# Kernel tuning notes

Hardware: AMD Instinct MI355X
Metric: run time of the kernel (lower is better)

Reference implementation:

```python
import jax, jax.numpy as jnp
import numpy as np

B, T, C, H = 8, 1024, 512, 8


def setup_inputs() -> dict:
    key = jax.random.key(0)
    k1, k2, k3, k4 = jax.random.split(key, 4)
    x = jax.random.normal(k1, (B, T, C), jnp.float32)
    q = jax.random.normal(k2, (B, T, C), jnp.float32)
    W_kv = jax.random.normal(k3, (C, 2 * C), jnp.float32) * 0.02
    W_proj = jax.random.normal(k4, (C, C), jnp.float32) * 0.02
    return {"x": x, "q": q, "W_kv": W_kv, "W_proj": W_proj}


def reference(x, q, W_kv, W_proj):
    B, T, C = x.shape
    H = 8
    D = C // H
    T2 = T // 2
    # kv projection (nn.Linear, no bias)
    kv = x @ W_kv                      # [B,T,2C]
    k, v = kv[..., :C], kv[..., C:]
    # 7 batch-dim rolls of the first half, then reinterpret [7,B,T2,C] -> [B,7*T2,C]
    # (exactly what torch.stack(...).view(B,-1,C) does on the contiguous buffer)
    sk = jnp.stack([jnp.roll(k[:, :T2], i, axis=0) for i in range(7)]).reshape(B, -1, C)
    sv = jnp.stack([jnp.roll(v[:, :T2], i, axis=0) for i in range(7)]).reshape(B, -1, C)
    k = jnp.concatenate((sk, k), axis=1)   # [B, S, C], S = 7*T2 + T
    v = jnp.concatenate((sv, v), axis=1)
    qh = q.reshape(B, T, H, D).transpose(0, 2, 1, 3)    # [B,H,T,D]
    kh = k.reshape(B, -1, H, D).transpose(0, 2, 1, 3)   # [B,H,S,D]
    vh = v.reshape(B, -1, H, D).transpose(0, 2, 1, 3)   # [B,H,S,D]
    scale = 1.0 / jnp.sqrt(jnp.float32(D))
    # NOTE: the torch module passes attn_mask=None to SDPA, so attention is unmasked
    scores = jnp.einsum('bhld,bhsd->bhls', qh, kh) * scale
    attn = jax.nn.softmax(scores, axis=-1)
    y = jnp.einsum('bhls,bhsd->bhld', attn, vh)
    y = y.transpose(0, 2, 1, 3).reshape(B, T, C)
    return y @ W_proj
```

## Files before the change

kernel.cpp:

```cpp
#include <hip/hip_runtime.h>

typedef __bf16 bf16;
typedef bf16 bf16x8 __attribute__((ext_vector_type(8)));
typedef bf16 bf16x4 __attribute__((ext_vector_type(4)));
typedef float f32x4 __attribute__((ext_vector_type(4)));
typedef float f32x16 __attribute__((ext_vector_type(16)));
typedef unsigned int u32;

#define DEV_INLINE __device__ __forceinline__

DEV_INLINE f32x4 mfma16(bf16x8 a, bf16x8 b, f32x4 c) {
    return __builtin_amdgcn_mfma_f32_16x16x32_bf16(a, b, c, 0, 0, 0);
}
DEV_INLINE f32x16 mfma32(bf16x8 a, bf16x8 b, f32x16 c) {
    return __builtin_amdgcn_mfma_f32_32x32x16_bf16(a, b, c, 0, 0, 0);
}

#define GLD16(gp, lp) __builtin_amdgcn_global_load_lds( \
    (const __attribute__((address_space(1))) void*)(gp), \
    (__attribute__((address_space(3))) void*)(lp), 16, 0, 0)

__global__ void transpose_cast_kernel(const float* __restrict__ in, bf16* __restrict__ out,
                                      int K, int N) {
    int idx = blockIdx.x * blockDim.x + threadIdx.x;
    if (idx < K * N) {
        int n = idx / K, k = idx - n * K;
        out[idx] = (bf16)in[k * N + n];
    }
}

__launch_bounds__(256, 2)
__global__ void gemm_kv_kernel(const float* __restrict__ A,
                               const bf16* __restrict__ Bt,
                               bf16* __restrict__ Kout,
                               bf16* __restrict__ Vt)
{
    __shared__ bf16 As[128][32];
    __shared__ bf16 Bs[128][32];
    const int bm = blockIdx.x, bn = blockIdx.y;
    const int tid = threadIdx.x;
    const int lane = tid & 63, w = tid >> 6;
    const int wm = (w >> 1) * 64, wn = (w & 1) * 64;
    const int lr = lane & 15, kg = lane >> 4;

    const f32x4 fz = {0.f, 0.f, 0.f, 0.f};
    f32x4 acc[4][4];
    for (int i = 0; i < 4; ++i)
        for (int j = 0; j < 4; ++j) acc[i][j] = fz;

    const int srow = tid >> 2, sc4 = tid & 3;

    for (int k0 = 0; k0 < 512; k0 += 32) {
        __syncthreads();
        for (int rr = 0; rr < 2; ++rr) {
            int row = srow + rr * 64;
            const float* ap = A + (size_t)(bm * 128 + row) * 512 + k0 + (sc4 << 3);
            f32x4 a0 = *reinterpret_cast<const f32x4*>(ap);
            f32x4 a1 = *reinterpret_cast<const f32x4*>(ap + 4);
            bf16x8 av;
            for (int j = 0; j < 4; ++j) { av[j] = (bf16)a0[j]; av[4 + j] = (bf16)a1[j]; }
            *reinterpret_cast<bf16x8*>(&As[row][(sc4 ^ (row & 3)) << 3]) = av;
            *reinterpret_cast<bf16x8*>(&Bs[row][(sc4 ^ (row & 3)) << 3]) =
                *reinterpret_cast<const bf16x8*>(Bt + (size_t)(bn * 128 + row) * 512 + k0 + (sc4 << 3));
        }
        __syncthreads();
        bf16x8 af[4], bfr[4];
        for (int mi = 0; mi < 4; ++mi) {
            int row = wm + mi * 16 + lr;
            af[mi] = *reinterpret_cast<const bf16x8*>(&As[row][(kg ^ (row & 3)) << 3]);
        }
        for (int ni = 0; ni < 4; ++ni) {
            int row = wn + ni * 16 + lr;
            bfr[ni] = *reinterpret_cast<const bf16x8*>(&Bs[row][(kg ^ (row & 3)) << 3]);
        }
        for (int mi = 0; mi < 4; ++mi)
            for (int ni = 0; ni < 4; ++ni)
                acc[mi][ni] = mfma16(af[mi], bfr[ni], acc[mi][ni]);
    }

    for (int mi = 0; mi < 4; ++mi) {
        int mbase = bm * 128 + wm + mi * 16 + kg * 4;
        for (int ni = 0; ni < 4; ++ni) {
            int col = bn * 128 + wn + ni * 16 + lr;
            if (col < 512) {
                for (int r = 0; r < 4; ++r)
                    Kout[(size_t)(mbase + r) * 512 + col] = (bf16)acc[mi][ni][r];
            } else {
                int c = col - 512, h = c >> 6, d = c & 63;
                int b = mbase >> 10, t = mbase & 1023;
                int tp = (t & ~12) | ((t & 4) << 1) | ((t & 8) >> 1);
                bf16x4 pk;
                for (int r = 0; r < 4; ++r) pk[r] = (bf16)acc[mi][ni][r];
                *reinterpret_cast<bf16x4*>(Vt + (size_t)((b * 8 + h) * 64 + d) * 1024 + tp) = pk;
            }
        }
    }
}

__launch_bounds__(256, 2)
__global__ void gemm_proj_kernel(const bf16* __restrict__ A,
                                 const bf16* __restrict__ Bt,
                                 float* __restrict__ out)
{
    __shared__ bf16 As[128][32];
    __shared__ bf16 Bs[128][32];
    const int bm = blockIdx.x, bn = blockIdx.y;
    const int tid = threadIdx.x;
    const int lane = tid & 63, w = tid >> 6;
    const int wm = (w >> 1) * 64, wn = (w & 1) * 64;
    const int lr = lane & 15, kg = lane >> 4;

    const f32x4 fz = {0.f, 0.f, 0.f, 0.f};
    f32x4 acc[4][4];
    for (int i = 0; i < 4; ++i)
        for (int j = 0; j < 4; ++j) acc[i][j] = fz;

    const int srow = tid >> 2, sc4 = tid & 3;

    for (int k0 = 0; k0 < 512; k0 += 32) {
        __syncthreads();
        for (int rr = 0; rr < 2; ++rr) {
            int row = srow + rr * 64;
            *reinterpret_cast<bf16x8*>(&As[row][(sc4 ^ (row & 3)) << 3]) =
                *reinterpret_cast<const bf16x8*>(A + (size_t)(bm * 128 + row) * 512 + k0 + (sc4 << 3));
            *reinterpret_cast<bf16x8*>(&Bs[row][(sc4 ^ (row & 3)) << 3]) =
                *reinterpret_cast<const bf16x8*>(Bt + (size_t)(bn * 128 + row) * 512 + k0 + (sc4 << 3));
        }
        __syncthreads();
        bf16x8 af[4], bfr[4];
        for (int mi = 0; mi < 4; ++mi) {
            int row = wm + mi * 16 + lr;
            af[mi] = *reinterpret_cast<const bf16x8*>(&As[row][(kg ^ (row & 3)) << 3]);
        }
        for (int ni = 0; ni < 4; ++ni) {
            int row = wn + ni * 16 + lr;
            bfr[ni] = *reinterpret_cast<const bf16x8*>(&Bs[row][(kg ^ (row & 3)) << 3]);
        }
        for (int mi = 0; mi < 4; ++mi)
            for (int ni = 0; ni < 4; ++ni)
                acc[mi][ni] = mfma16(af[mi], bfr[ni], acc[mi][ni]);
    }

    for (int mi = 0; mi < 4; ++mi) {
        int mbase = bm * 128 + wm + mi * 16 + kg * 4;
        for (int ni = 0; ni < 4; ++ni) {
            int col = bn * 128 + wn + ni * 16 + lr;
            for (int r = 0; r < 4; ++r)
                out[(size_t)(mbase + r) * 512 + col] = acc[mi][ni][r];
        }
    }
}

__launch_bounds__(512, 2)
__global__ void attn_kernel(const float* __restrict__ Qr,
                            const bf16* __restrict__ Kb,
                            const bf16* __restrict__ Vt,
                            bf16* __restrict__ Op,
                            float* __restrict__ Lp)
{
    __shared__ bf16 sK[2][64][64];
    __shared__ bf16 sV[2][64][64];

    const int raw = blockIdx.x;
    const int h = raw & 7;
    const int shalf = (raw >> 3) & 1;
    const int qseg = (raw >> 4) & 3;
    const int b = raw >> 6;
    const int tid = threadIdx.x, lane = tid & 63, w = tid >> 6;
    const int lq = lane & 31, hi = lane >> 5;
    const int qrow = b * 1024 + qseg * 256 + w * 32 + lq;
    const int sbase = shalf * 2304;

    const float QSC = 0.18033688011112306f;
    bf16x8 qf[4];
#pragma unroll
    for (int ds = 0; ds < 4; ++ds) {
        const float* qp = Qr + (size_t)qrow * 512 + h * 64 + ds * 16 + hi * 8;
        f32x4 q0 = *reinterpret_cast<const f32x4*>(qp);
        f32x4 q1 = *reinterpret_cast<const f32x4*>(qp + 4);
#pragma unroll
        for (int j = 0; j < 4; ++j) {
            qf[ds][j]     = (bf16)(q0[j] * QSC);
            qf[ds][4 + j] = (bf16)(q1[j] * QSC);
        }
    }

    const f32x16 Z16 = {0,0,0,0,0,0,0,0,0,0,0,0,0,0,0,0};
    f32x16 O0 = Z16, O1 = Z16, lv = Z16;

    const bf16* Kf = &sK[0][0][0];
    const bf16* Vf = &sV[0][0][0];
    int koffE[4], voffE[4];
#pragma unroll
    for (int ds = 0; ds < 4; ++ds) {
        koffE[ds] = lq * 64 + (((ds * 2 + hi) ^ (lq & 7)) * 8);
        voffE[ds] = lq * 64 + (((ds * 2 + hi) ^ (lq & 7)) * 8);
    }

    const int srow = w * 8 + (lane >> 3);
    const int schunk = (lane & 7) ^ (srow & 7);
    const size_t koff = (size_t)srow * 512 + schunk * 8;
    const size_t voff = (size_t)srow * 1024 + schunk * 8;

    auto kv_base = [&](int t, const bf16*& kp, const bf16*& vp) {
        int gs = sbase + t * 64;
        int jj = gs >> 9, tin = gs & 511;
        if (jj < 7) {
            int m7 = 7 * b + jj;
            int src_b = ((m7 & 7) - (m7 >> 3)) & 7;
            kp = Kb + (size_t)(src_b * 1024 + tin) * 512 + h * 64;
            vp = Vt + (size_t)((src_b * 8 + h) * 64) * 1024 + tin;
        } else {
            int tpos = (jj - 7) * 512 + tin;
            kp = Kb + (size_t)(b * 1024 + tpos) * 512 + h * 64;
            vp = Vt + (size_t)((b * 8 + h) * 64) * 1024 + tpos;
        }
    };

    auto stage = [&](int buf, int t) {
        const bf16 *kp, *vp;
        kv_base(t, kp, vp);
        GLD16(kp + koff, &sK[buf][w * 8][0]);
        GLD16(vp + voff, &sV[buf][w * 8][0]);
    };

    auto computeTile = [&](int cb) {
        const int kb = cb * 4096;
        f32x16 s0, s1;
        __builtin_amdgcn_s_setprio(1);
        {
            bf16x8 k0 = *reinterpret_cast<const bf16x8*>(Kf + kb + koffE[0]);
            bf16x8 k1 = *reinterpret_cast<const bf16x8*>(Kf + kb + 2048 + koffE[0]);
            s0 = mfma32(k0, qf[0], Z16);
            s1 = mfma32(k1, qf[0], Z16);
        }
#pragma unroll
        for (int ds = 1; ds < 4; ++ds) {
            bf16x8 k0 = *reinterpret_cast<const bf16x8*>(Kf + kb + koffE[ds]);
            bf16x8 k1 = *reinterpret_cast<const bf16x8*>(Kf + kb + 2048 + koffE[ds]);
            s0 = mfma32(k0, qf[ds], s0);
            s1 = mfma32(k1, qf[ds], s1);
        }
        __builtin_amdgcn_s_setprio(0);

#pragma unroll
        for (int i = 0; i < 16; ++i) {
            float p0 = __builtin_amdgcn_exp2f(s0[i]); s0[i] = p0;
            float p1 = __builtin_amdgcn_exp2f(s1[i]); s1[i] = p1;
            lv[i] += p0 + p1;
        }

        __builtin_amdgcn_s_setprio(1);
#pragma unroll
        for (int ssub = 0; ssub < 4; ++ssub) {
            bf16x8 pf;
#pragma unroll
            for (int i = 0; i < 8; ++i) {
                float pv = (ssub < 2) ? ((ssub & 1) ? s0[8 + i] : s0[i])
                                      : ((ssub & 1) ? s1[8 + i] : s1[i]);
                pf[i] = (bf16)pv;
            }
            bf16x8 a0 = *reinterpret_cast<const bf16x8*>(Vf + kb + voffE[ssub]);
            bf16x8 a1 = *reinterpret_cast<const bf16x8*>(Vf + kb + 2048 + voffE[ssub]);
            O0 = mfma32(a0, pf, O0);
            O1 = mfma32(a1, pf, O1);
        }
        __builtin_amdgcn_s_setprio(0);
    };

    stage(0, 0);

    for (int t = 0; t < 36; t += 2) {
        __syncthreads();
        stage(1, t + 1);
        computeTile(0);
        __syncthreads();
        if (t + 2 < 36) stage(0, t + 2);
        computeTile(1);
    }

    float lrun = 0.f;
#pragma unroll
    for (int i = 0; i < 16; ++i) lrun += lv[i];
    lrun += __shfl_xor(lrun, 32);
    if (hi == 0) Lp[shalf * 65536 + h * 8192 + qrow] = lrun;

    bf16* Od = Op + (size_t)shalf * 4194304;
#pragma unroll
    for (int dh = 0; dh < 2; ++dh) {
#pragma unroll
        for (int q4 = 0; q4 < 4; ++q4) {
            bf16x4 pk;
#pragma unroll
            for (int i = 0; i < 4; ++i)
                pk[i] = (bf16)(dh ? O1[q4 * 4 + i] : O0[q4 * 4 + i]);
            *reinterpret_cast<bf16x4*>(
                Od + (size_t)qrow * 512 + h * 64 + dh * 32 + q4 * 8 + hi * 4) = pk;
        }
    }
}

__global__ void combine_kernel(const bf16* __restrict__ Op, const float* __restrict__ Lp,
                               bf16* __restrict__ Y) {
    int i = blockIdx.x * blockDim.x + threadIdx.x;
    int row = i >> 6;
    int col8 = (i & 63) * 8;
    int h = col8 >> 6;
    float l = Lp[h * 8192 + row] + Lp[65536 + h * 8192 + row];
    float inv = 1.0f / l;
    size_t off = (size_t)row * 512 + col8;
    bf16x8 a = *reinterpret_cast<const bf16x8*>(Op + off);
    bf16x8 c = *reinterpret_cast<const bf16x8*>(Op + 4194304 + off);
    bf16x8 o;
#pragma unroll
    for (int j = 0; j < 8; ++j)
        o[j] = (bf16)(((float)a[j] + (float)c[j]) * inv);
    *reinterpret_cast<bf16x8*>(Y + off) = o;
}

extern "C" void kernel_launch(void* const* d_in, const int* in_sizes, int n_in,
                              void* d_out, int out_size, void* d_ws, size_t ws_size,
                              hipStream_t stream) {
    const float* x   = (const float*)d_in[0];
    const float* q   = (const float*)d_in[1];
    const float* Wkv = (const float*)d_in[2];
    const float* Wp  = (const float*)d_in[3];
    float* out = (float*)d_out;

    char* ws = (char*)d_ws;
    bf16*  Kb   = (bf16*)(ws);
    bf16*  Vt   = (bf16*)(ws + 8388608);
    bf16*  Opar = (bf16*)(ws + 16777216);
    bf16*  Yb   = (bf16*)(ws + 33554432);
    bf16*  Wkvt = (bf16*)(ws + 41943040);
    bf16*  Wpt  = (bf16*)(ws + 42991616);
    float* Lp   = (float*)(ws + 43515904);

    transpose_cast_kernel<<<(512 * 1024) / 256, 256, 0, stream>>>(Wkv, Wkvt, 512, 1024);
    transpose_cast_kernel<<<(512 * 512) / 256, 256, 0, stream>>>(Wp, Wpt, 512, 512);
    gemm_kv_kernel<<<dim3(64, 8), 256, 0, stream>>>(x, Wkvt, Kb, Vt);
    attn_kernel<<<512, 512, 0, stream>>>(q, Kb, Vt, Opar, Lp);
    combine_kernel<<<(8192 * 512 / 8) / 256, 256, 0, stream>>>(Opar, Lp, Yb);
    gemm_proj_kernel<<<dim3(64, 4), 256, 0, stream>>>(Yb, Wpt, out);
}
```

Baseline: 126.6 us.

## Process two query tiles per attention wave and fuse combine into projection GEMM

Each attention wave now handles 64 query rows (two 32-row MFMA tiles) that share the same K/V fragments read from LDS. The block shrinks to 256 threads, and each thread stages twice as many K/V rows. This halves LDS fragment reads per query and doubles register pressure for the accumulators. Separately, the combine kernel is removed: its normalisation and sum of the two split-S partials happen while the A tile is loaded in the projection GEMM. That saves one launch and a round trip through the Y buffer, but the merge is recomputed by each of the four column blocks.

```diff
diff --git a/kernel.cpp b/kernel.cpp
--- a/kernel.cpp
+++ b/kernel.cpp
@@ -4,6 +4,7 @@
 typedef bf16 bf16x8 __attribute__((ext_vector_type(8)));
 typedef bf16 bf16x4 __attribute__((ext_vector_type(4)));
 typedef float f32x4 __attribute__((ext_vector_type(4)));
+typedef float f32x8 __attribute__((ext_vector_type(8)));
 typedef float f32x16 __attribute__((ext_vector_type(16)));
 typedef unsigned int u32;
 
@@ -98,7 +99,8 @@
 }
 
 __launch_bounds__(256, 2)
-__global__ void gemm_proj_kernel(const bf16* __restrict__ A,
+__global__ void gemm_proj_kernel(const bf16* __restrict__ Op,
+                                 const float* __restrict__ Lp,
                                  const bf16* __restrict__ Bt,
                                  float* __restrict__ out)
 {
@@ -121,8 +123,18 @@
         __syncthreads();
         for (int rr = 0; rr < 2; ++rr) {
             int row = srow + rr * 64;
-            *reinterpret_cast<bf16x8*>(&As[row][(sc4 ^ (row & 3)) << 3]) =
-                *reinterpret_cast<const bf16x8*>(A + (size_t)(bm * 128 + row) * 512 + k0 + (sc4 << 3));
+            int grow = bm * 128 + row;
+            int kc = k0 + (sc4 << 3);
+            int hh = kc >> 6;
+            float l = Lp[hh * 8192 + grow] + Lp[65536 + hh * 8192 + grow];
+            float inv = 1.0f / l;
+            size_t off = (size_t)grow * 512 + kc;
+            bf16x8 a = *reinterpret_cast<const bf16x8*>(Op + off);
+            bf16x8 c = *reinterpret_cast<const bf16x8*>(Op + 4194304 + off);
+            bf16x8 av;
+            for (int j = 0; j < 8; ++j)
+                av[j] = (bf16)(((float)a[j] + (float)c[j]) * inv);
+            *reinterpret_cast<bf16x8*>(&As[row][(sc4 ^ (row & 3)) << 3]) = av;
             *reinterpret_cast<bf16x8*>(&Bs[row][(sc4 ^ (row & 3)) << 3]) =
                 *reinterpret_cast<const bf16x8*>(Bt + (size_t)(bn * 128 + row) * 512 + k0 + (sc4 << 3));
         }
@@ -151,7 +163,7 @@
     }
 }
 
-__launch_bounds__(512, 2)
+__launch_bounds__(256, 2)
 __global__ void attn_kernel(const float* __restrict__ Qr,
                             const bf16* __restrict__ Kb,
                             const bf16* __restrict__ Vt,
@@ -168,25 +180,33 @@
     const int b = raw >> 6;
     const int tid = threadIdx.x, lane = tid & 63, w = tid >> 6;
     const int lq = lane & 31, hi = lane >> 5;
-    const int qrow = b * 1024 + qseg * 256 + w * 32 + lq;
+    const int qA = b * 1024 + qseg * 256 + w * 64 + lq;
+    const int qB = qA + 32;
     const int sbase = shalf * 2304;
 
     const float QSC = 0.18033688011112306f;
-    bf16x8 qf[4];
+    bf16x8 qfA[4], qfB[4];
 #pragma unroll
     for (int ds = 0; ds < 4; ++ds) {
-        const float* qp = Qr + (size_t)qrow * 512 + h * 64 + ds * 16 + hi * 8;
-        f32x4 q0 = *reinterpret_cast<const f32x4*>(qp);
-        f32x4 q1 = *reinterpret_cast<const f32x4*>(qp + 4);
+        const float* qpA = Qr + (size_t)qA * 512 + h * 64 + ds * 16 + hi * 8;
+        const float* qpB = Qr + (size_t)qB * 512 + h * 64 + ds * 16 + hi * 8;
+        f32x4 a0 = *reinterpret_cast<const f32x4*>(qpA);
+        f32x4 a1 = *reinterpret_cast<const f32x4*>(qpA + 4);
+        f32x4 b0 = *reinterpret_cast<const f32x4*>(qpB);
+        f32x4 b1 = *reinterpret_cast<const f32x4*>(qpB + 4);
 #pragma unroll
         for (int j = 0; j < 4; ++j) {
-            qf[ds][j]     = (bf16)(q0[j] * QSC);
-            qf[ds][4 + j] = (bf16)(q1[j] * QSC);
+            qfA[ds][j]     = (bf16)(a0[j] * QSC);
+            qfA[ds][4 + j] = (bf16)(a1[j] * QSC);
+            qfB[ds][j]     = (bf16)(b0[j] * QSC);
+            qfB[ds][4 + j] = (bf16)(b1[j] * QSC);
         }
     }
 
     const f32x16 Z16 = {0,0,0,0,0,0,0,0,0,0,0,0,0,0,0,0};
-    f32x16 O0 = Z16, O1 = Z16, lv = Z16;
+    const f32x8 Z8 = {0,0,0,0,0,0,0,0};
+    f32x16 O0a = Z16, O1a = Z16, O0b = Z16, O1b = Z16;
+    f32x8 lvA = Z8, lvB = Z8;
 
     const bf16* Kf = &sK[0][0][0];
     const bf16* Vf = &sV[0][0][0];
@@ -197,8 +217,8 @@
         voffE[ds] = lq * 64 + (((ds * 2 + hi) ^ (lq & 7)) * 8);
     }
 
-    const int srow = w * 8 + (lane >> 3);
-    const int schunk = (lane & 7) ^ (srow & 7);
+    const int srow = w * 16 + (lane >> 3);
+    const int schunk = (lane & 7) ^ ((lane >> 3) & 7);
     const size_t koff = (size_t)srow * 512 + schunk * 8;
     const size_t voff = (size_t)srow * 1024 + schunk * 8;
 
@@ -220,50 +240,64 @@
     auto stage = [&](int buf, int t) {
         const bf16 *kp, *vp;
         kv_base(t, kp, vp);
-        GLD16(kp + koff, &sK[buf][w * 8][0]);
-        GLD16(vp + voff, &sV[buf][w * 8][0]);
+        GLD16(kp + koff,            &sK[buf][w * 16][0]);
+        GLD16(kp + koff + 8 * 512,  &sK[buf][w * 16 + 8][0]);
+        GLD16(vp + voff,            &sV[buf][w * 16][0]);
+        GLD16(vp + voff + 8 * 1024, &sV[buf][w * 16 + 8][0]);
     };
 
     auto computeTile = [&](int cb) {
         const int kb = cb * 4096;
-        f32x16 s0, s1;
+        f32x16 sa0, sa1, sb0, sb1;
         __builtin_amdgcn_s_setprio(1);
         {
             bf16x8 k0 = *reinterpret_cast<const bf16x8*>(Kf + kb + koffE[0]);
             bf16x8 k1 = *reinterpret_cast<const bf16x8*>(Kf + kb + 2048 + koffE[0]);
-            s0 = mfma32(k0, qf[0], Z16);
-            s1 = mfma32(k1, qf[0], Z16);
+            sa0 = mfma32(k0, qfA[0], Z16); sa1 = mfma32(k1, qfA[0], Z16);
+            sb0 = mfma32(k0, qfB[0], Z16); sb1 = mfma32(k1, qfB[0], Z16);
         }
 #pragma unroll
         for (int ds = 1; ds < 4; ++ds) {
             bf16x8 k0 = *reinterpret_cast<const bf16x8*>(Kf + kb + koffE[ds]);
             bf16x8 k1 = *reinterpret_cast<const bf16x8*>(Kf + kb + 2048 + koffE[ds]);
-            s0 = mfma32(k0, qf[ds], s0);
-            s1 = mfma32(k1, qf[ds], s1);
+            sa0 = mfma32(k0, qfA[ds], sa0); sa1 = mfma32(k1, qfA[ds], sa1);
+            sb0 = mfma32(k0, qfB[ds], sb0); sb1 = mfma32(k1, qfB[ds], sb1);
         }
         __builtin_amdgcn_s_setprio(0);
 
+        bf16x8 pA[4], pB[4];
 #pragma unroll
         for (int i = 0; i < 16; ++i) {
-            float p0 = __builtin_amdgcn_exp2f(s0[i]); s0[i] = p0;
-            float p1 = __builtin_amdgcn_exp2f(s1[i]); s1[i] = p1;
-            lv[i] += p0 + p1;
-        }
+            float p0 = __builtin_amdgcn_exp2f(sa0[i]); sa0[i] = p0;
+            float p1 = __builtin_amdgcn_exp2f(sa1[i]); sa1[i] = p1;
+            lvA[i & 7] += p0 + p1;
+        }
+#pragma unroll
+        for (int ssub = 0; ssub < 4; ++ssub)
+#pragma unroll
+            for (int i = 0; i < 8; ++i)
+                pA[ssub][i] = (bf16)((ssub < 2) ? ((ssub & 1) ? sa0[8 + i] : sa0[i])
+                                                : ((ssub & 1) ? sa1[8 + i] : sa1[i]));
+#pragma unroll
+        for (int i = 0; i < 16; ++i) {
+            float p0 = __builtin_amdgcn_exp2f(sb0[i]); sb0[i] = p0;
+            float p1 = __builtin_amdgcn_exp2f(sb1[i]); sb1[i] = p1;
+            lvB[i & 7] += p0 + p1;
+        }
+#pragma unroll
+        for (int ssub = 0; ssub < 4; ++ssub)
+#pragma unroll
+            for (int i = 0; i < 8; ++i)
+                pB[ssub][i] = (bf16)((ssub < 2) ? ((ssub & 1) ? sb0[8 + i] : sb0[i])
+                                                : ((ssub & 1) ? sb1[8 + i] : sb1[i]));
 
         __builtin_amdgcn_s_setprio(1);
 #pragma unroll
         for (int ssub = 0; ssub < 4; ++ssub) {
-            bf16x8 pf;
-#pragma unroll
-            for (int i = 0; i < 8; ++i) {
-                float pv = (ssub < 2) ? ((ssub & 1) ? s0[8 + i] : s0[i])
-                                      : ((ssub & 1) ? s1[8 + i] : s1[i]);
-                pf[i] = (bf16)pv;
-            }
             bf16x8 a0 = *reinterpret_cast<const bf16x8*>(Vf + kb + voffE[ssub]);
             bf16x8 a1 = *reinterpret_cast<const bf16x8*>(Vf + kb + 2048 + voffE[ssub]);
-            O0 = mfma32(a0, pf, O0);
-            O1 = mfma32(a1, pf, O1);
+            O0a = mfma32(a0, pA[ssub], O0a); O1a = mfma32(a1, pA[ssub], O1a);
+            O0b = mfma32(a0, pB[ssub], O0b); O1b = mfma32(a1, pB[ssub], O1b);
         }
         __builtin_amdgcn_s_setprio(0);
     };
@@ -279,43 +313,33 @@
         computeTile(1);
     }
 
-    float lrun = 0.f;
-#pragma unroll
-    for (int i = 0; i < 16; ++i) lrun += lv[i];
-    lrun += __shfl_xor(lrun, 32);
-    if (hi == 0) Lp[shalf * 65536 + h * 8192 + qrow] = lrun;
+    float lA = 0.f, lB = 0.f;
+#pragma unroll
+    for (int i = 0; i < 8; ++i) { lA += lvA[i]; lB += lvB[i]; }
+    lA += __shfl_xor(lA, 32);
+    lB += __shfl_xor(lB, 32);
+    if (hi == 0) {
+        Lp[shalf * 65536 + h * 8192 + qA] = lA;
+        Lp[shalf * 65536 + h * 8192 + qB] = lB;
+    }
 
     bf16* Od = Op + (size_t)shalf * 4194304;
 #pragma unroll
     for (int dh = 0; dh < 2; ++dh) {
 #pragma unroll
         for (int q4 = 0; q4 < 4; ++q4) {
-            bf16x4 pk;
-#pragma unroll
-            for (int i = 0; i < 4; ++i)
-                pk[i] = (bf16)(dh ? O1[q4 * 4 + i] : O0[q4 * 4 + i]);
+            bf16x4 pka, pkb;
+#pragma unroll
+            for (int i = 0; i < 4; ++i) {
+                pka[i] = (bf16)(dh ? O1a[q4 * 4 + i] : O0a[q4 * 4 + i]);
+                pkb[i] = (bf16)(dh ? O1b[q4 * 4 + i] : O0b[q4 * 4 + i]);
+            }
             *reinterpret_cast<bf16x4*>(
-                Od + (size_t)qrow * 512 + h * 64 + dh * 32 + q4 * 8 + hi * 4) = pk;
-        }
-    }
-}
-
-__global__ void combine_kernel(const bf16* __restrict__ Op, const float* __restrict__ Lp,
-                               bf16* __restrict__ Y) {
-    int i = blockIdx.x * blockDim.x + threadIdx.x;
-    int row = i >> 6;
-    int col8 = (i & 63) * 8;
-    int h = col8 >> 6;
-    float l = Lp[h * 8192 + row] + Lp[65536 + h * 8192 + row];
-    float inv = 1.0f / l;
-    size_t off = (size_t)row * 512 + col8;
-    bf16x8 a = *reinterpret_cast<const bf16x8*>(Op + off);
-    bf16x8 c = *reinterpret_cast<const bf16x8*>(Op + 4194304 + off);
-    bf16x8 o;
-#pragma unroll
-    for (int j = 0; j < 8; ++j)
-        o[j] = (bf16)(((float)a[j] + (float)c[j]) * inv);
-    *reinterpret_cast<bf16x8*>(Y + off) = o;
+                Od + (size_t)qA * 512 + h * 64 + dh * 32 + q4 * 8 + hi * 4) = pka;
+            *reinterpret_cast<bf16x4*>(
+                Od + (size_t)qB * 512 + h * 64 + dh * 32 + q4 * 8 + hi * 4) = pkb;
+        }
+    }
 }
 
 extern "C" void kernel_launch(void* const* d_in, const int* in_sizes, int n_in,
@@ -331,7 +355,6 @@
     bf16*  Kb   = (bf16*)(ws);
     bf16*  Vt   = (bf16*)(ws + 8388608);
     bf16*  Opar = (bf16*)(ws + 16777216);
-    bf16*  Yb   = (bf16*)(ws + 33554432);
     bf16*  Wkvt = (bf16*)(ws + 41943040);
     bf16*  Wpt  = (bf16*)(ws + 42991616);
     float* Lp   = (float*)(ws + 43515904);
@@ -339,7 +362,6 @@
     transpose_cast_kernel<<<(512 * 1024) / 256, 256, 0, stream>>>(Wkv, Wkvt, 512, 1024);
     transpose_cast_kernel<<<(512 * 512) / 256, 256, 0, stream>>>(Wp, Wpt, 512, 512);
     gemm_kv_kernel<<<dim3(64, 8), 256, 0, stream>>>(x, Wkvt, Kb, Vt);
-    attn_kernel<<<512, 512, 0, stream>>>(q, Kb, Vt, Opar, Lp);
-    combine_kernel<<<(8192 * 512 / 8) / 256, 256, 0, stream>>>(Opar, Lp, Yb);
-    gemm_proj_kernel<<<dim3(64, 4), 256, 0, stream>>>(Yb, Wpt, out);
-}
+    attn_kernel<<<512, 256, 0, stream>>>(q, Kb, Vt, Opar, Lp);
+    gemm_proj_kernel<<<dim3(64, 4), 256, 0, stream>>>(Opar, Lp, Wpt, out);
+}
```

Measured after the change: 128.4 us. No clear change (+1.4%).
